# Kernel optimization log

Measured on AMD Instinct MI355X. Metric: run time of the kernel, lower is better.

## Reference

```python
import jax, jax.numpy as jnp
import numpy as np

B, S, H, DEPTH = 2, 2048, 8, 64
D_MODEL = H * DEPTH  # 512


def setup_inputs() -> dict:
    key = jax.random.key(0)
    ks = jax.random.split(key, 6)
    s = 0.02
    return {
        "emb_x": jax.random.normal(ks[0], (B, S, D_MODEL), dtype=jnp.float32),
        "pe_rel_t": jax.random.normal(ks[1], (B, S, D_MODEL), dtype=jnp.float32),
        "Wq": jax.random.normal(ks[2], (D_MODEL, D_MODEL), dtype=jnp.float32) * s,
        "bq": jnp.zeros((D_MODEL,), dtype=jnp.float32),
        "Wk": jax.random.normal(ks[3], (D_MODEL, D_MODEL), dtype=jnp.float32) * s,
        "bk": jnp.zeros((D_MODEL,), dtype=jnp.float32),
        "Wv": jax.random.normal(ks[4], (D_MODEL, D_MODEL), dtype=jnp.float32) * s,
        "bv": jnp.zeros((D_MODEL,), dtype=jnp.float32),
        "Wo": jax.random.normal(ks[5], (D_MODEL, D_MODEL), dtype=jnp.float32) * s,
        "bo": jnp.zeros((D_MODEL,), dtype=jnp.float32),
    }


def _split_heads(x):
    # [B, S, D_MODEL] -> [B, H, S, DEPTH]
    b, s, _ = x.shape
    return x.reshape(b, s, H, DEPTH).transpose(0, 2, 1, 3)


def reference(emb_x, pe_rel_t, Wq, bq, Wk, bk, Wv, bv, Wo, bo):
    # RPE attention: content and relative-position streams share WQ/WK.
    Q_c = _split_heads(emb_x @ Wq + bq)
    Q_r = _split_heads(pe_rel_t @ Wq + bq)
    K_c = _split_heads(emb_x @ Wk + bk)
    K_r = _split_heads(pe_rel_t @ Wk + bk)
    V_c = _split_heads(emb_x @ Wv + bv)

    logits = (
        jnp.einsum("bhqd,bhkd->bhqk", Q_c, K_c)
        + jnp.einsum("bhqd,bhkd->bhqk", Q_r, K_c)
        + jnp.einsum("bhqd,bhkd->bhqk", Q_c, K_r)
    ) / jnp.sqrt(jnp.asarray(DEPTH, dtype=emb_x.dtype))

    attn = jax.nn.softmax(logits, axis=-1)  # [B, H, S, S]
    z = jnp.einsum("bhqk,bhkd->bhqd", attn, V_c)  # [B, H, S, DEPTH]
    z = z.transpose(0, 2, 1, 3).reshape(emb_x.shape[0], -1, D_MODEL)
    out = z @ Wo + bo
    return out, attn
```

## Files before the change

kernel.cpp:

```cpp
#include <hip/hip_runtime.h>
#include <hip/hip_bf16.h>


typedef __bf16 bf16;
typedef bf16 bf16x4 __attribute__((ext_vector_type(4)));
typedef bf16 bf16x8 __attribute__((ext_vector_type(8)));
typedef float f32x4 __attribute__((ext_vector_type(4)));

#define B_ 2
#define S_ 2048
#define H_ 8
#define D_ 64
#define DM_ 512
#define M_ 4096

__global__ __launch_bounds__(256) void pack_x(const float4* __restrict__ emb,
                                              const float4* __restrict__ pe,
                                              bf16* __restrict__ xb,
                                              bf16* __restrict__ xp,
                                              bf16* __restrict__ xs) {
    int i = blockIdx.x * 256 + threadIdx.x;
    float4 a = emb[i], b = pe[i];
    int o = i * 4;
    bf16x4 va, vp, vs;
    va.x = (bf16)a.x; va.y = (bf16)a.y; va.z = (bf16)a.z; va.w = (bf16)a.w;
    vp.x = (bf16)b.x; vp.y = (bf16)b.y; vp.z = (bf16)b.z; vp.w = (bf16)b.w;
    vs.x = (bf16)(a.x + b.x); vs.y = (bf16)(a.y + b.y);
    vs.z = (bf16)(a.z + b.z); vs.w = (bf16)(a.w + b.w);
    *(bf16x4*)(xb + o) = va;
    *(bf16x4*)(xp + o) = vp;
    *(bf16x4*)(xs + o) = vs;
}

__global__ __launch_bounds__(256) void pack_w(const float* __restrict__ W,
                                              bf16* __restrict__ WT) {
    int idx = blockIdx.x * 256 + threadIdx.x;
    int n = idx >> 9, k = idx & 511;
    WT[idx] = (bf16)W[k * 512 + n];
}

template <int AMODE, int SMODE>
__global__ __launch_bounds__(256) void proj_gemm(const bf16* __restrict__ A,
                                                 const bf16* __restrict__ BT,
                                                 const float* __restrict__ bias,
                                                 float bscale,
                                                 void* __restrict__ Cout) {
    __shared__ bf16 As[64][72];
    __shared__ bf16 Bs[64][72];
    const int tid = threadIdx.x;
    const int lane = tid & 63;
    const int wave = tid >> 6;
    const int wm = wave >> 1, wn = wave & 1;
    const int row0 = blockIdx.x * 64;
    const int col0 = blockIdx.y * 64;
    const int lm = lane & 15, lk = (lane >> 4) * 8;

    f32x4 acc[2][2] = {{{0.f,0.f,0.f,0.f},{0.f,0.f,0.f,0.f}},
                       {{0.f,0.f,0.f,0.f},{0.f,0.f,0.f,0.f}}};

    for (int k0 = 0; k0 < 512; k0 += 64) {
        for (int i = 0; i < 2; ++i) {
            int idx = tid + i * 256;
            int r = idx >> 3, sg = (idx & 7) * 8;
            long aoff;
            int arow = row0 + r, acol = k0 + sg;
            if (AMODE == 0) {
                aoff = (long)arow * 512 + acol;
            } else {
                int b = arow >> 11, s = arow & 2047, h = acol >> 6, d = acol & 63;
                aoff = (((long)(b * H_ + h) * S_ + s) * 64) + d;
            }
            *(bf16x8*)&As[r][sg] = *(const bf16x8*)(A + aoff);
            *(bf16x8*)&Bs[r][sg] = *(const bf16x8*)(BT + (long)(col0 + r) * 512 + k0 + sg);
        }
        __syncthreads();
        for (int kk = 0; kk < 64; kk += 32) {
            bf16x8 af[2], bfr[2];
            for (int t = 0; t < 2; ++t) {
                af[t]  = *(const bf16x8*)&As[wm * 32 + t * 16 + lm][kk + lk];
                bfr[t] = *(const bf16x8*)&Bs[wn * 32 + t * 16 + lm][kk + lk];
            }
            for (int mt = 0; mt < 2; ++mt)
                for (int nt = 0; nt < 2; ++nt)
                    acc[mt][nt] = __builtin_amdgcn_mfma_f32_16x16x32_bf16(
                        af[mt], bfr[nt], acc[mt][nt], 0, 0, 0);
        }
        __syncthreads();
    }

    const int rbase = (lane >> 4) * 4;
    for (int mt = 0; mt < 2; ++mt)
        for (int nt = 0; nt < 2; ++nt)
            for (int r = 0; r < 4; ++r) {
                int row = row0 + wm * 32 + mt * 16 + rbase + r;
                int col = col0 + wn * 32 + nt * 16 + lm;
                float v = acc[mt][nt][r] + bias[col] * bscale;
                int b = row >> 11, s = row & 2047, h = col >> 6, d = col & 63;
                if (SMODE == 0) {
                    ((bf16*)Cout)[(((long)(b * H_ + h) * S_ + s) * 64) + d] = (bf16)v;
                } else if (SMODE == 1) {
                    ((bf16*)Cout)[(((long)(b * H_ + h) * 64 + d) * S_) + s] = (bf16)v;
                } else {
                    ((float*)Cout)[(long)row * 512 + col] = v;
                }
            }
}

__global__ __launch_bounds__(256) void attn_kernel(const bf16* __restrict__ Qc,
                                                   const bf16* __restrict__ Qr,
                                                   const bf16* __restrict__ Kc,
                                                   const bf16* __restrict__ Ks,
                                                   const bf16* __restrict__ Vt,
                                                   bf16* __restrict__ Zb,
                                                   float* __restrict__ attn_out) {
    __shared__ bf16 Kcs[64][72];
    __shared__ bf16 Kss[64][72];
    __shared__ bf16 Vts[64][72];
    __shared__ bf16 ptile[4][16][40];

    const int tid = threadIdx.x, lane = tid & 63, wave = tid >> 6;
    const int bh = blockIdx.x >> 5;
    const int qt = blockIdx.x & 31;
    const int qw = qt * 64 + wave * 16;
    const long kbase = (long)bh * (S_ * 64);
    const long vbase = (long)bh * (64 * S_);
    const int lm = lane & 15, lk = (lane >> 4) * 8;
    const float SC = 0.125f;

    bf16x8 qcf[2], qrf[2];
    for (int kt = 0; kt < 2; ++kt) {
        long off = kbase + (long)(qw + lm) * 64 + kt * 32 + lk;
        qcf[kt] = *(const bf16x8*)(Qc + off);
        qrf[kt] = *(const bf16x8*)(Qr + off);
    }

    float rsum[4] = {0.f, 0.f, 0.f, 0.f};
    f32x4 zacc[4] = {{0.f,0.f,0.f,0.f},{0.f,0.f,0.f,0.f},
                     {0.f,0.f,0.f,0.f},{0.f,0.f,0.f,0.f}};

    for (int key0 = 0; key0 < S_; key0 += 64) {
        __syncthreads();
        for (int i = 0; i < 2; ++i) {
            int idx = tid + i * 256, r = idx >> 3, sg = (idx & 7) * 8;
            *(bf16x8*)&Kcs[r][sg] = *(const bf16x8*)(Kc + kbase + (long)(key0 + r) * 64 + sg);
            *(bf16x8*)&Kss[r][sg] = *(const bf16x8*)(Ks + kbase + (long)(key0 + r) * 64 + sg);
            *(bf16x8*)&Vts[r][sg] = *(const bf16x8*)(Vt + vbase + (long)r * S_ + key0 + sg);
        }
        __syncthreads();
        for (int pair = 0; pair < 2; ++pair) {
            for (int nt = 0; nt < 2; ++nt) {
                const int keyl = pair * 32 + nt * 16;
                f32x4 acc = {0.f, 0.f, 0.f, 0.f};
                for (int kt = 0; kt < 2; ++kt) {
                    bf16x8 bs = *(const bf16x8*)&Kss[keyl + lm][kt * 32 + lk];
                    bf16x8 bc = *(const bf16x8*)&Kcs[keyl + lm][kt * 32 + lk];
                    acc = __builtin_amdgcn_mfma_f32_16x16x32_bf16(qcf[kt], bs, acc, 0, 0, 0);
                    acc = __builtin_amdgcn_mfma_f32_16x16x32_bf16(qrf[kt], bc, acc, 0, 0, 0);
                }
                for (int r = 0; r < 4; ++r) {
                    float p = __expf(acc[r] * SC);
                    rsum[r] += p;
                    ptile[wave][(lane >> 4) * 4 + r][nt * 16 + lm] = (bf16)p;
                }
            }
            __syncthreads();
            bf16x8 pa = *(const bf16x8*)&ptile[wave][lm][lk];
            for (int nt = 0; nt < 4; ++nt) {
                bf16x8 vb = *(const bf16x8*)&Vts[nt * 16 + lm][pair * 32 + lk];
                zacc[nt] = __builtin_amdgcn_mfma_f32_16x16x32_bf16(pa, vb, zacc[nt], 0, 0, 0);
            }
        }
    }

    float inv_r[4];
    for (int r = 0; r < 4; ++r) {
        float s = rsum[r];
        s += __shfl_xor(s, 1);
        s += __shfl_xor(s, 2);
        s += __shfl_xor(s, 4);
        s += __shfl_xor(s, 8);
        inv_r[r] = 1.0f / s;
    }

    for (int nt = 0; nt < 4; ++nt)
        for (int r = 0; r < 4; ++r)
            Zb[kbase + (long)(qw + (lane >> 4) * 4 + r) * 64 + nt * 16 + lm] =
                (bf16)(zacc[nt][r] * inv_r[r]);

    const long abase = (long)bh * S_ * S_;
    for (int key0 = 0; key0 < S_; key0 += 64) {
        __syncthreads();
        for (int i = 0; i < 2; ++i) {
            int idx = tid + i * 256, r = idx >> 3, sg = (idx & 7) * 8;
            *(bf16x8*)&Kcs[r][sg] = *(const bf16x8*)(Kc + kbase + (long)(key0 + r) * 64 + sg);
            *(bf16x8*)&Kss[r][sg] = *(const bf16x8*)(Ks + kbase + (long)(key0 + r) * 64 + sg);
        }
        __syncthreads();
        for (int nt = 0; nt < 4; ++nt) {
            const int keyl = nt * 16;
            f32x4 acc = {0.f, 0.f, 0.f, 0.f};
            for (int kt = 0; kt < 2; ++kt) {
                bf16x8 bs = *(const bf16x8*)&Kss[keyl + lm][kt * 32 + lk];
                bf16x8 bc = *(const bf16x8*)&Kcs[keyl + lm][kt * 32 + lk];
                acc = __builtin_amdgcn_mfma_f32_16x16x32_bf16(qcf[kt], bs, acc, 0, 0, 0);
                acc = __builtin_amdgcn_mfma_f32_16x16x32_bf16(qrf[kt], bc, acc, 0, 0, 0);
            }
            for (int r = 0; r < 4; ++r) {
                float p = __expf(acc[r] * SC) * inv_r[r];
                attn_out[abase + (long)(qw + (lane >> 4) * 4 + r) * S_ + key0 + keyl + lm] = p;
            }
        }
    }
}

extern "C" void kernel_launch(void* const* d_in, const int* in_sizes, int n_in,
                              void* d_out, int out_size, void* d_ws, size_t ws_size,
                              hipStream_t stream) {
    const float* emb = (const float*)d_in[0];
    const float* pe  = (const float*)d_in[1];
    const float* Wq  = (const float*)d_in[2];
    const float* bq  = (const float*)d_in[3];
    const float* Wk  = (const float*)d_in[4];
    const float* bk  = (const float*)d_in[5];
    const float* Wv  = (const float*)d_in[6];
    const float* bv  = (const float*)d_in[7];
    const float* Wo  = (const float*)d_in[8];
    const float* bo  = (const float*)d_in[9];

    float* outp = (float*)d_out;
    float* attn = outp + (long)B_ * S_ * DM_;

    char* w = (char*)d_ws;
    const long SZ_X = (long)M_ * DM_ * 2;
    const long SZ_W = (long)DM_ * DM_ * 2;
    bf16* Xb  = (bf16*)(w);
    bf16* Xp  = (bf16*)(w + SZ_X);
    bf16* Xs  = (bf16*)(w + 2 * SZ_X);
    bf16* WqT = (bf16*)(w + 3 * SZ_X);
    bf16* WkT = (bf16*)(w + 3 * SZ_X + SZ_W);
    bf16* WvT = (bf16*)(w + 3 * SZ_X + 2 * SZ_W);
    bf16* WoT = (bf16*)(w + 3 * SZ_X + 3 * SZ_W);
    char* p2  = w + 3 * SZ_X + 4 * SZ_W;
    bf16* Qc  = (bf16*)(p2);
    bf16* Qr  = (bf16*)(p2 + SZ_X);
    bf16* Kc  = (bf16*)(p2 + 2 * SZ_X);
    bf16* Ks  = (bf16*)(p2 + 3 * SZ_X);
    bf16* Vt  = (bf16*)(p2 + 4 * SZ_X);
    bf16* Zb  = (bf16*)(p2 + 5 * SZ_X);

    pack_x<<<(M_ * DM_ / 4) / 256, 256, 0, stream>>>(
        (const float4*)emb, (const float4*)pe, Xb, Xp, Xs);
    pack_w<<<(DM_ * DM_) / 256, 256, 0, stream>>>(Wq, WqT);
    pack_w<<<(DM_ * DM_) / 256, 256, 0, stream>>>(Wk, WkT);
    pack_w<<<(DM_ * DM_) / 256, 256, 0, stream>>>(Wv, WvT);
    pack_w<<<(DM_ * DM_) / 256, 256, 0, stream>>>(Wo, WoT);

    dim3 g(M_ / 64, DM_ / 64);
    proj_gemm<0, 0><<<g, 256, 0, stream>>>(Xb, WqT, bq, 1.f, Qc);
    proj_gemm<0, 0><<<g, 256, 0, stream>>>(Xp, WqT, bq, 1.f, Qr);
    proj_gemm<0, 0><<<g, 256, 0, stream>>>(Xb, WkT, bk, 1.f, Kc);
    proj_gemm<0, 0><<<g, 256, 0, stream>>>(Xs, WkT, bk, 2.f, Ks);
    proj_gemm<0, 1><<<g, 256, 0, stream>>>(Xb, WvT, bv, 1.f, Vt);

    attn_kernel<<<B_ * H_ * (S_ / 64), 256, 0, stream>>>(
        Qc, Qr, Kc, Ks, Vt, Zb, attn);

    proj_gemm<1, 2><<<g, 256, 0, stream>>>(Zb, WoT, bo, 1.f, (void*)outp);
}
```

Measured before the change: 429.8 us.

## Batch projection launches, tile weight transpose, and register-prefetch K/V tiles

```diff
diff --git a/kernel.cpp b/kernel.cpp
--- a/kernel.cpp
+++ b/kernel.cpp
@@ -32,19 +32,104 @@
     *(bf16x4*)(xs + o) = vs;
 }
 
-__global__ __launch_bounds__(256) void pack_w(const float* __restrict__ W,
-                                              bf16* __restrict__ WT) {
-    int idx = blockIdx.x * 256 + threadIdx.x;
-    int n = idx >> 9, k = idx & 511;
-    WT[idx] = (bf16)W[k * 512 + n];
-}
-
-template <int AMODE, int SMODE>
-__global__ __launch_bounds__(256) void proj_gemm(const bf16* __restrict__ A,
-                                                 const bf16* __restrict__ BT,
-                                                 const float* __restrict__ bias,
-                                                 float bscale,
-                                                 void* __restrict__ Cout) {
+__global__ __launch_bounds__(256) void pack_w4(const float* __restrict__ Wq,
+                                               const float* __restrict__ Wk,
+                                               const float* __restrict__ Wv,
+                                               const float* __restrict__ Wo,
+                                               bf16* __restrict__ WT) {
+    __shared__ float t[32][33];
+    const float* W = (blockIdx.z == 0) ? Wq : (blockIdx.z == 1) ? Wk
+                   : (blockIdx.z == 2) ? Wv : Wo;
+    bf16* dst = WT + (long)blockIdx.z * (DM_ * DM_);
+    const int r = threadIdx.x >> 5, c = threadIdx.x & 31;
+    const int kb = blockIdx.x * 32, nb = blockIdx.y * 32;
+    for (int i = 0; i < 4; ++i)
+        t[r + 8 * i][c] = W[(long)(kb + r + 8 * i) * 512 + nb + c];
+    __syncthreads();
+    for (int i = 0; i < 4; ++i)
+        dst[(long)(nb + r + 8 * i) * 512 + kb + c] = (bf16)t[c][r + 8 * i];
+}
+
+__global__ __launch_bounds__(256) void proj_fused(
+    const bf16* __restrict__ Xb, const bf16* __restrict__ Xp,
+    const bf16* __restrict__ Xs, const bf16* __restrict__ WT,
+    const float* __restrict__ bq, const float* __restrict__ bk,
+    const float* __restrict__ bv,
+    bf16* __restrict__ Qc, bf16* __restrict__ Qr, bf16* __restrict__ Kc,
+    bf16* __restrict__ Ks, bf16* __restrict__ Vt) {
+    __shared__ bf16 As[64][72];
+    __shared__ bf16 Bs[64][72];
+
+    const int z = blockIdx.z;
+    const bf16* A = (z == 1) ? Xp : (z == 3) ? Xs : Xb;
+    const bf16* BT = WT + (long)(z >> 1) * (DM_ * DM_);
+    const float* bias = (z >= 4) ? bv : (z >= 2) ? bk : bq;
+    const float bscale = (z == 3) ? 2.f : 1.f;
+    bf16* dst = (z == 0) ? Qc : (z == 1) ? Qr : (z == 2) ? Kc
+              : (z == 3) ? Ks : Vt;
+    const bool vmode = (z == 4);
+
+    const int tid = threadIdx.x;
+    const int lane = tid & 63;
+    const int wave = tid >> 6;
+    const int wm = wave >> 1, wn = wave & 1;
+    const int row0 = blockIdx.x * 64;
+    const int col0 = blockIdx.y * 64;
+    const int lm = lane & 15, lk = (lane >> 4) * 8;
+    const int r0 = tid >> 3, sg0 = (tid & 7) * 8;
+
+    f32x4 acc[2][2] = {{{0.f,0.f,0.f,0.f},{0.f,0.f,0.f,0.f}},
+                       {{0.f,0.f,0.f,0.f},{0.f,0.f,0.f,0.f}}};
+
+    bf16x8 ra[2], rb[2];
+    auto load_ab = [&](int k0) {
+        ra[0] = *(const bf16x8*)(A + (long)(row0 + r0) * 512 + k0 + sg0);
+        ra[1] = *(const bf16x8*)(A + (long)(row0 + r0 + 32) * 512 + k0 + sg0);
+        rb[0] = *(const bf16x8*)(BT + (long)(col0 + r0) * 512 + k0 + sg0);
+        rb[1] = *(const bf16x8*)(BT + (long)(col0 + r0 + 32) * 512 + k0 + sg0);
+    };
+
+    load_ab(0);
+    for (int k0 = 0; k0 < 512; k0 += 64) {
+        *(bf16x8*)&As[r0][sg0]      = ra[0];
+        *(bf16x8*)&As[r0 + 32][sg0] = ra[1];
+        *(bf16x8*)&Bs[r0][sg0]      = rb[0];
+        *(bf16x8*)&Bs[r0 + 32][sg0] = rb[1];
+        __syncthreads();
+        if (k0 < 448) load_ab(k0 + 64);
+        for (int kk = 0; kk < 64; kk += 32) {
+            bf16x8 af[2], bfr[2];
+            for (int t = 0; t < 2; ++t) {
+                af[t]  = *(const bf16x8*)&As[wm * 32 + t * 16 + lm][kk + lk];
+                bfr[t] = *(const bf16x8*)&Bs[wn * 32 + t * 16 + lm][kk + lk];
+            }
+            for (int mt = 0; mt < 2; ++mt)
+                for (int nt = 0; nt < 2; ++nt)
+                    acc[mt][nt] = __builtin_amdgcn_mfma_f32_16x16x32_bf16(
+                        af[mt], bfr[nt], acc[mt][nt], 0, 0, 0);
+        }
+        __syncthreads();
+    }
+
+    const int rbase = (lane >> 4) * 4;
+    for (int mt = 0; mt < 2; ++mt)
+        for (int nt = 0; nt < 2; ++nt)
+            for (int r = 0; r < 4; ++r) {
+                int row = row0 + wm * 32 + mt * 16 + rbase + r;
+                int col = col0 + wn * 32 + nt * 16 + lm;
+                float v = acc[mt][nt][r] + bias[col] * bscale;
+                int b = row >> 11, s = row & 2047, h = col >> 6, d = col & 63;
+                if (!vmode)
+                    dst[(((long)(b * H_ + h) * S_ + s) * 64) + d] = (bf16)v;
+                else
+                    dst[(((long)(b * H_ + h) * 64 + d) * S_) + s] = (bf16)v;
+            }
+}
+
+__global__ __launch_bounds__(256) void proj_out(const bf16* __restrict__ Zb,
+                                                const bf16* __restrict__ WoT,
+                                                const float* __restrict__ bo,
+                                                float* __restrict__ Out) {
     __shared__ bf16 As[64][72];
     __shared__ bf16 Bs[64][72];
     const int tid = threadIdx.x;
@@ -54,26 +139,37 @@
     const int row0 = blockIdx.x * 64;
     const int col0 = blockIdx.y * 64;
     const int lm = lane & 15, lk = (lane >> 4) * 8;
+    const int r0 = tid >> 3, sg0 = (tid & 7) * 8;
 
     f32x4 acc[2][2] = {{{0.f,0.f,0.f,0.f},{0.f,0.f,0.f,0.f}},
                        {{0.f,0.f,0.f,0.f},{0.f,0.f,0.f,0.f}}};
 
+    bf16x8 ra[2], rb[2];
+    auto load_ab = [&](int k0) {
+        const int acol = k0 + sg0;
+        const int h = acol >> 6, d = acol & 63;
+        {
+            int arow = row0 + r0;
+            int b = arow >> 11, s = arow & 2047;
+            ra[0] = *(const bf16x8*)(Zb + (((long)(b * H_ + h) * S_ + s) * 64) + d);
+        }
+        {
+            int arow = row0 + r0 + 32;
+            int b = arow >> 11, s = arow & 2047;
+            ra[1] = *(const bf16x8*)(Zb + (((long)(b * H_ + h) * S_ + s) * 64) + d);
+        }
+        rb[0] = *(const bf16x8*)(WoT + (long)(col0 + r0) * 512 + k0 + sg0);
+        rb[1] = *(const bf16x8*)(WoT + (long)(col0 + r0 + 32) * 512 + k0 + sg0);
+    };
+
+    load_ab(0);
     for (int k0 = 0; k0 < 512; k0 += 64) {
-        for (int i = 0; i < 2; ++i) {
-            int idx = tid + i * 256;
-            int r = idx >> 3, sg = (idx & 7) * 8;
-            long aoff;
-            int arow = row0 + r, acol = k0 + sg;
-            if (AMODE == 0) {
-                aoff = (long)arow * 512 + acol;
-            } else {
-                int b = arow >> 11, s = arow & 2047, h = acol >> 6, d = acol & 63;
-                aoff = (((long)(b * H_ + h) * S_ + s) * 64) + d;
-            }
-            *(bf16x8*)&As[r][sg] = *(const bf16x8*)(A + aoff);
-            *(bf16x8*)&Bs[r][sg] = *(const bf16x8*)(BT + (long)(col0 + r) * 512 + k0 + sg);
-        }
-        __syncthreads();
+        *(bf16x8*)&As[r0][sg0]      = ra[0];
+        *(bf16x8*)&As[r0 + 32][sg0] = ra[1];
+        *(bf16x8*)&Bs[r0][sg0]      = rb[0];
+        *(bf16x8*)&Bs[r0 + 32][sg0] = rb[1];
+        __syncthreads();
+        if (k0 < 448) load_ab(k0 + 64);
         for (int kk = 0; kk < 64; kk += 32) {
             bf16x8 af[2], bfr[2];
             for (int t = 0; t < 2; ++t) {
@@ -94,15 +190,7 @@
             for (int r = 0; r < 4; ++r) {
                 int row = row0 + wm * 32 + mt * 16 + rbase + r;
                 int col = col0 + wn * 32 + nt * 16 + lm;
-                float v = acc[mt][nt][r] + bias[col] * bscale;
-                int b = row >> 11, s = row & 2047, h = col >> 6, d = col & 63;
-                if (SMODE == 0) {
-                    ((bf16*)Cout)[(((long)(b * H_ + h) * S_ + s) * 64) + d] = (bf16)v;
-                } else if (SMODE == 1) {
-                    ((bf16*)Cout)[(((long)(b * H_ + h) * 64 + d) * S_) + s] = (bf16)v;
-                } else {
-                    ((float*)Cout)[(long)row * 512 + col] = v;
-                }
+                Out[(long)row * 512 + col] = acc[mt][nt][r] + bo[col];
             }
 }
 
@@ -125,6 +213,7 @@
     const long kbase = (long)bh * (S_ * 64);
     const long vbase = (long)bh * (64 * S_);
     const int lm = lane & 15, lk = (lane >> 4) * 8;
+    const int r0 = tid >> 3, sg0 = (tid & 7) * 8;
     const float SC = 0.125f;
 
     bf16x8 qcf[2], qrf[2];
@@ -138,15 +227,28 @@
     f32x4 zacc[4] = {{0.f,0.f,0.f,0.f},{0.f,0.f,0.f,0.f},
                      {0.f,0.f,0.f,0.f},{0.f,0.f,0.f,0.f}};
 
+    bf16x8 rk[2], rs[2], rv[2];
+    auto load_kv = [&](int key0) {
+        rk[0] = *(const bf16x8*)(Kc + kbase + (long)(key0 + r0) * 64 + sg0);
+        rk[1] = *(const bf16x8*)(Kc + kbase + (long)(key0 + r0 + 32) * 64 + sg0);
+        rs[0] = *(const bf16x8*)(Ks + kbase + (long)(key0 + r0) * 64 + sg0);
+        rs[1] = *(const bf16x8*)(Ks + kbase + (long)(key0 + r0 + 32) * 64 + sg0);
+        rv[0] = *(const bf16x8*)(Vt + vbase + (long)r0 * S_ + key0 + sg0);
+        rv[1] = *(const bf16x8*)(Vt + vbase + (long)(r0 + 32) * S_ + key0 + sg0);
+    };
+
+    load_kv(0);
     for (int key0 = 0; key0 < S_; key0 += 64) {
         __syncthreads();
-        for (int i = 0; i < 2; ++i) {
-            int idx = tid + i * 256, r = idx >> 3, sg = (idx & 7) * 8;
-            *(bf16x8*)&Kcs[r][sg] = *(const bf16x8*)(Kc + kbase + (long)(key0 + r) * 64 + sg);
-            *(bf16x8*)&Kss[r][sg] = *(const bf16x8*)(Ks + kbase + (long)(key0 + r) * 64 + sg);
-            *(bf16x8*)&Vts[r][sg] = *(const bf16x8*)(Vt + vbase + (long)r * S_ + key0 + sg);
-        }
-        __syncthreads();
+        *(bf16x8*)&Kcs[r0][sg0]      = rk[0];
+        *(bf16x8*)&Kcs[r0 + 32][sg0] = rk[1];
+        *(bf16x8*)&Kss[r0][sg0]      = rs[0];
+        *(bf16x8*)&Kss[r0 + 32][sg0] = rs[1];
+        *(bf16x8*)&Vts[r0][sg0]      = rv[0];
+        *(bf16x8*)&Vts[r0 + 32][sg0] = rv[1];
+        __syncthreads();
+        if (key0 + 64 < S_) load_kv(key0 + 64);
+
         for (int pair = 0; pair < 2; ++pair) {
             for (int nt = 0; nt < 2; ++nt) {
                 const int keyl = pair * 32 + nt * 16;
@@ -163,7 +265,6 @@
                     ptile[wave][(lane >> 4) * 4 + r][nt * 16 + lm] = (bf16)p;
                 }
             }
-            __syncthreads();
             bf16x8 pa = *(const bf16x8*)&ptile[wave][lm][lk];
             for (int nt = 0; nt < 4; ++nt) {
                 bf16x8 vb = *(const bf16x8*)&Vts[nt * 16 + lm][pair * 32 + lk];
@@ -182,6 +283,14 @@
         inv_r[r] = 1.0f / s;
     }
 
+    auto load_k = [&](int key0) {
+        rk[0] = *(const bf16x8*)(Kc + kbase + (long)(key0 + r0) * 64 + sg0);
+        rk[1] = *(const bf16x8*)(Kc + kbase + (long)(key0 + r0 + 32) * 64 + sg0);
+        rs[0] = *(const bf16x8*)(Ks + kbase + (long)(key0 + r0) * 64 + sg0);
+        rs[1] = *(const bf16x8*)(Ks + kbase + (long)(key0 + r0 + 32) * 64 + sg0);
+    };
+    load_k(0);
+
     for (int nt = 0; nt < 4; ++nt)
         for (int r = 0; r < 4; ++r)
             Zb[kbase + (long)(qw + (lane >> 4) * 4 + r) * 64 + nt * 16 + lm] =
@@ -190,12 +299,13 @@
     const long abase = (long)bh * S_ * S_;
     for (int key0 = 0; key0 < S_; key0 += 64) {
         __syncthreads();
-        for (int i = 0; i < 2; ++i) {
-            int idx = tid + i * 256, r = idx >> 3, sg = (idx & 7) * 8;
-            *(bf16x8*)&Kcs[r][sg] = *(const bf16x8*)(Kc + kbase + (long)(key0 + r) * 64 + sg);
-            *(bf16x8*)&Kss[r][sg] = *(const bf16x8*)(Ks + kbase + (long)(key0 + r) * 64 + sg);
-        }
-        __syncthreads();
+        *(bf16x8*)&Kcs[r0][sg0]      = rk[0];
+        *(bf16x8*)&Kcs[r0 + 32][sg0] = rk[1];
+        *(bf16x8*)&Kss[r0][sg0]      = rs[0];
+        *(bf16x8*)&Kss[r0 + 32][sg0] = rs[1];
+        __syncthreads();
+        if (key0 + 64 < S_) load_k(key0 + 64);
+
         for (int nt = 0; nt < 4; ++nt) {
             const int keyl = nt * 16;
             f32x4 acc = {0.f, 0.f, 0.f, 0.f};
@@ -237,8 +347,6 @@
     bf16* Xp  = (bf16*)(w + SZ_X);
     bf16* Xs  = (bf16*)(w + 2 * SZ_X);
     bf16* WqT = (bf16*)(w + 3 * SZ_X);
-    bf16* WkT = (bf16*)(w + 3 * SZ_X + SZ_W);
-    bf16* WvT = (bf16*)(w + 3 * SZ_X + 2 * SZ_W);
     bf16* WoT = (bf16*)(w + 3 * SZ_X + 3 * SZ_W);
     char* p2  = w + 3 * SZ_X + 4 * SZ_W;
     bf16* Qc  = (bf16*)(p2);
@@ -250,20 +358,13 @@
 
     pack_x<<<(M_ * DM_ / 4) / 256, 256, 0, stream>>>(
         (const float4*)emb, (const float4*)pe, Xb, Xp, Xs);
-    pack_w<<<(DM_ * DM_) / 256, 256, 0, stream>>>(Wq, WqT);
-    pack_w<<<(DM_ * DM_) / 256, 256, 0, stream>>>(Wk, WkT);
-    pack_w<<<(DM_ * DM_) / 256, 256, 0, stream>>>(Wv, WvT);
-    pack_w<<<(DM_ * DM_) / 256, 256, 0, stream>>>(Wo, WoT);
-
-    dim3 g(M_ / 64, DM_ / 64);
-    proj_gemm<0, 0><<<g, 256, 0, stream>>>(Xb, WqT, bq, 1.f, Qc);
-    proj_gemm<0, 0><<<g, 256, 0, stream>>>(Xp, WqT, bq, 1.f, Qr);
-    proj_gemm<0, 0><<<g, 256, 0, stream>>>(Xb, WkT, bk, 1.f, Kc);
-    proj_gemm<0, 0><<<g, 256, 0, stream>>>(Xs, WkT, bk, 2.f, Ks);
-    proj_gemm<0, 1><<<g, 256, 0, stream>>>(Xb, WvT, bv, 1.f, Vt);
+    pack_w4<<<dim3(16, 16, 4), 256, 0, stream>>>(Wq, Wk, Wv, Wo, WqT);
+
+    proj_fused<<<dim3(M_ / 64, DM_ / 64, 5), 256, 0, stream>>>(
+        Xb, Xp, Xs, WqT, bq, bk, bv, Qc, Qr, Kc, Ks, Vt);
 
     attn_kernel<<<B_ * H_ * (S_ / 64), 256, 0, stream>>>(
         Qc, Qr, Kc, Ks, Vt, Zb, attn);
 
-    proj_gemm<1, 2><<<g, 256, 0, stream>>>(Zb, WoT, bo, 1.f, (void*)outp);
-}
+    proj_out<<<dim3(M_ / 64, DM_ / 64), 256, 0, stream>>>(Zb, WoT, bo, outp);
+}
```

New measurement: 420.3 us. 1.02x faster.
